# Performance work log

Hardware: AMD Instinct MI355X
Metric: run time of the kernel (lower is better)

Reference implementation:

```python
import jax, jax.numpy as jnp
import numpy as np

N_NODES = 100000
N_EDGES = 1600000
NODE_DIM = 5
HIDDEN = 64
N_LAYERS = 3


def setup_inputs() -> dict:
    key = jax.random.key(0)
    ks = jax.random.split(key, 12)
    s = 0.1
    return {
        "x": jax.random.normal(ks[0], (N_NODES, NODE_DIM), dtype=jnp.float32),
        "edge_index": jax.random.randint(ks[1], (2, N_EDGES), 0, N_NODES, dtype=jnp.int32),
        # message MLP params per layer (stacked over layers)
        "W1": jax.random.normal(ks[2], (N_LAYERS, 2 * NODE_DIM, HIDDEN), dtype=jnp.float32) * s,
        "b1": jnp.zeros((N_LAYERS, HIDDEN), dtype=jnp.float32),
        "W2": jax.random.normal(ks[3], (N_LAYERS, HIDDEN, NODE_DIM), dtype=jnp.float32) * s,
        "b2": jnp.zeros((N_LAYERS, NODE_DIM), dtype=jnp.float32),
        # update MLP params per layer
        "U1": jax.random.normal(ks[4], (N_LAYERS, 2 * NODE_DIM, HIDDEN), dtype=jnp.float32) * s,
        "bu1": jnp.zeros((N_LAYERS, HIDDEN), dtype=jnp.float32),
        "U2": jax.random.normal(ks[5], (N_LAYERS, HIDDEN, NODE_DIM), dtype=jnp.float32) * s,
        "bu2": jnp.zeros((N_LAYERS, NODE_DIM), dtype=jnp.float32),
        # readout
        "Wr": jax.random.normal(ks[6], (NODE_DIM, NODE_DIM), dtype=jnp.float32) * s,
        "br": jnp.zeros((NODE_DIM,), dtype=jnp.float32),
    }


def reference(x, edge_index, W1, b1, W2, b2, U1, bu1, U2, bu2, Wr, br):
    # PyG convention: messages flow from source j = edge_index[0] to target i = edge_index[1]
    src = edge_index[0]
    dst = edge_index[1]
    n = x.shape[0]
    for l in range(N_LAYERS):
        x_i = x[dst]                                   # [E, d] target features
        x_j = x[src]                                   # [E, d] source features
        msg_in = jnp.concatenate([x_i, x_j], axis=-1)  # [E, 2d]
        msg = jax.nn.relu(msg_in @ W1[l] + b1[l]) @ W2[l] + b2[l]   # [E, d]
        aggr = jax.ops.segment_sum(msg, dst, num_segments=n)        # [N, d] scatter-add at targets
        upd_in = jnp.concatenate([x, aggr], axis=-1)   # [N, 2d]
        upd = jax.nn.relu(upd_in @ U1[l] + bu1[l]) @ U2[l] + bu2[l]  # [N, d]
        x = upd + x                                    # residual (in SkeletonGNN.forward)
    return x @ Wr + br
```

## Files before the change

### kernel.cpp

```cpp
#include <hip/hip_runtime.h>

#define N_NODES 100000
#define N_EDGES 1600000
#define DIM 5
#define HID 64
#define N_LAYERS 3
#define SCAN_BLK 256
#define NBLK ((N_NODES + SCAN_BLK - 1) / SCAN_BLK)


__global__ __launch_bounds__(256) void hist_kernel(
    const int* __restrict__ ei, int* __restrict__ cnt, int* __restrict__ rank)
{
    int e = blockIdx.x * blockDim.x + threadIdx.x;
    if (e >= N_EDGES) return;
    int dst = ei[N_EDGES + e];
    rank[e] = atomicAdd(&cnt[dst], 1);
}

__global__ __launch_bounds__(SCAN_BLK) void scan_part_kernel(
    const int* __restrict__ cnt, int* __restrict__ blk_sum)
{
    __shared__ int s[SCAN_BLK];
    int t = threadIdx.x;
    int i = blockIdx.x * SCAN_BLK + t;
    s[t] = (i < N_NODES) ? cnt[i] : 0;
    __syncthreads();
    for (int off = SCAN_BLK / 2; off > 0; off >>= 1) {
        if (t < off) s[t] += s[t + off];
        __syncthreads();
    }
    if (t == 0) blk_sum[blockIdx.x] = s[0];
}

__global__ __launch_bounds__(512) void scan_blk_kernel(
    const int* __restrict__ blk_sum, int* __restrict__ blk_pref)
{
    __shared__ int s[512];
    int t = threadIdx.x;
    int v = (t < NBLK) ? blk_sum[t] : 0;
    s[t] = v;
    __syncthreads();
    for (int off = 1; off < 512; off <<= 1) {
        int a = (t >= off) ? s[t - off] : 0;
        __syncthreads();
        s[t] += a;
        __syncthreads();
    }
    if (t < NBLK) blk_pref[t] = s[t] - v;
}

__global__ __launch_bounds__(SCAN_BLK) void scan_add_kernel(
    const int* __restrict__ cnt, const int* __restrict__ blk_pref,
    int* __restrict__ row_ptr)
{
    __shared__ int s[SCAN_BLK];
    int t = threadIdx.x;
    int i = blockIdx.x * SCAN_BLK + t;
    int c = (i < N_NODES) ? cnt[i] : 0;
    s[t] = c;
    __syncthreads();
    for (int off = 1; off < SCAN_BLK; off <<= 1) {
        int a = (t >= off) ? s[t - off] : 0;
        __syncthreads();
        s[t] += a;
        __syncthreads();
    }
    if (i < N_NODES) row_ptr[i] = blk_pref[blockIdx.x] + s[t] - c;
    if (i == 0) row_ptr[N_NODES] = N_EDGES;
}

__global__ __launch_bounds__(256) void scatter_pair_kernel(
    const int* __restrict__ ei, const int* __restrict__ rank,
    const int* __restrict__ row_ptr, int2* __restrict__ spair)
{
    int e = blockIdx.x * blockDim.x + threadIdx.x;
    if (e >= N_EDGES) return;
    int src = ei[e];
    int dst = ei[N_EDGES + e];
    spair[row_ptr[dst] + rank[e]] = make_int2(src, dst);
}


__global__ __launch_bounds__(256) void edge_msg_sorted_kernel(
    const float* __restrict__ x,
    const int2* __restrict__ spair,
    const float* __restrict__ W1, const float* __restrict__ b1,
    const float* __restrict__ W2, const float* __restrict__ b2,
    float* __restrict__ msg_buf)
{
    int e = blockIdx.x * blockDim.x + threadIdx.x;
    if (e >= N_EDGES) return;
    int2 p = spair[e];

    float in[10];
    const float* xi = x + (long)p.y * DIM;
    const float* xj = x + (long)p.x * DIM;
#pragma unroll
    for (int d = 0; d < DIM; ++d) in[d] = xi[d];
#pragma unroll
    for (int d = 0; d < DIM; ++d) in[DIM + d] = xj[d];

    float msg[DIM];
#pragma unroll
    for (int j = 0; j < DIM; ++j) msg[j] = b2[j];

#pragma unroll 8
    for (int h = 0; h < HID; ++h) {
        float acc = b1[h];
#pragma unroll
        for (int d = 0; d < 10; ++d) acc = fmaf(in[d], W1[d * HID + h], acc);
        acc = fmaxf(acc, 0.0f);
#pragma unroll
        for (int j = 0; j < DIM; ++j) msg[j] = fmaf(acc, W2[h * DIM + j], msg[j]);
    }

    float* mp = msg_buf + (long)e * DIM;
#pragma unroll
    for (int j = 0; j < DIM; ++j) mp[j] = msg[j];
}

template <bool FINAL>
__global__ __launch_bounds__(256) void gather_update8_kernel(
    const float* __restrict__ x,
    const float* __restrict__ msg_buf,
    const int* __restrict__ row_ptr,
    const float* __restrict__ U1, const float* __restrict__ bu1,
    const float* __restrict__ U2, const float* __restrict__ bu2,
    const float* __restrict__ Wr, const float* __restrict__ br,
    float* __restrict__ xout)
{
    int gt = blockIdx.x * blockDim.x + threadIdx.x;
    int v = gt >> 3;
    int r = gt & 7;
    if (v >= N_NODES) return;

    int s = row_ptr[v], e1 = row_ptr[v + 1];

    float agg[DIM] = {0.f, 0.f, 0.f, 0.f, 0.f};
    for (int e = s + r; e < e1; e += 8) {
        const float* mp = msg_buf + (long)e * DIM;
#pragma unroll
        for (int j = 0; j < DIM; ++j) agg[j] += mp[j];
    }
#pragma unroll
    for (int m = 1; m < 8; m <<= 1) {
#pragma unroll
        for (int j = 0; j < DIM; ++j) agg[j] += __shfl_xor(agg[j], m, 64);
    }

    float in2[10];
#pragma unroll
    for (int d = 0; d < DIM; ++d) in2[d] = x[(long)v * DIM + d];
#pragma unroll
    for (int d = 0; d < DIM; ++d) in2[DIM + d] = agg[d];

    float upd[DIM] = {0.f, 0.f, 0.f, 0.f, 0.f};
#pragma unroll
    for (int hh = 0; hh < 8; ++hh) {
        int h = r + hh * 8;
        float acc = bu1[h];
#pragma unroll
        for (int d = 0; d < 10; ++d) acc = fmaf(in2[d], U1[d * HID + h], acc);
        acc = fmaxf(acc, 0.0f);
#pragma unroll
        for (int j = 0; j < DIM; ++j) upd[j] = fmaf(acc, U2[h * DIM + j], upd[j]);
    }
#pragma unroll
    for (int m = 1; m < 8; m <<= 1) {
#pragma unroll
        for (int j = 0; j < DIM; ++j) upd[j] += __shfl_xor(upd[j], m, 64);
    }

    if (r == 0) {
        float xn[DIM];
#pragma unroll
        for (int j = 0; j < DIM; ++j) xn[j] = upd[j] + bu2[j] + in2[j];
        if (FINAL) {
#pragma unroll
            for (int j = 0; j < DIM; ++j) {
                float o = br[j];
#pragma unroll
                for (int d = 0; d < DIM; ++d) o = fmaf(xn[d], Wr[d * DIM + j], o);
                xout[(long)v * DIM + j] = o;
            }
        } else {
#pragma unroll
            for (int j = 0; j < DIM; ++j) xout[(long)v * DIM + j] = xn[j];
        }
    }
}


__global__ __launch_bounds__(256) void edge_msg_kernel(
    const float* __restrict__ x, const int* __restrict__ ei,
    const float* __restrict__ W1, const float* __restrict__ b1,
    const float* __restrict__ W2, const float* __restrict__ b2,
    float* __restrict__ aggr)
{
    int e = blockIdx.x * blockDim.x + threadIdx.x;
    if (e >= N_EDGES) return;
    int src = ei[e];
    int dst = ei[N_EDGES + e];
    float in[10];
    const float* xi = x + (long)dst * DIM;
    const float* xj = x + (long)src * DIM;
#pragma unroll
    for (int d = 0; d < DIM; ++d) in[d] = xi[d];
#pragma unroll
    for (int d = 0; d < DIM; ++d) in[DIM + d] = xj[d];
    float msg[DIM];
#pragma unroll
    for (int j = 0; j < DIM; ++j) msg[j] = b2[j];
#pragma unroll 8
    for (int h = 0; h < HID; ++h) {
        float acc = b1[h];
#pragma unroll
        for (int d = 0; d < 10; ++d) acc = fmaf(in[d], W1[d * HID + h], acc);
        acc = fmaxf(acc, 0.0f);
#pragma unroll
        for (int j = 0; j < DIM; ++j) msg[j] = fmaf(acc, W2[h * DIM + j], msg[j]);
    }
    float* ap = aggr + (long)dst * DIM;
#pragma unroll
    for (int j = 0; j < DIM; ++j) atomicAdd(ap + j, msg[j]);
}

template <bool FINAL>
__global__ __launch_bounds__(256) void node_upd_kernel(
    const float* __restrict__ x, const float* __restrict__ aggr,
    const float* __restrict__ U1, const float* __restrict__ bu1,
    const float* __restrict__ U2, const float* __restrict__ bu2,
    const float* __restrict__ Wr, const float* __restrict__ br,
    float* __restrict__ xout)
{
    int v = blockIdx.x * blockDim.x + threadIdx.x;
    if (v >= N_NODES) return;
    float in[10];
#pragma unroll
    for (int d = 0; d < DIM; ++d) in[d] = x[(long)v * DIM + d];
#pragma unroll
    for (int d = 0; d < DIM; ++d) in[DIM + d] = aggr[(long)v * DIM + d];
    float upd[DIM];
#pragma unroll
    for (int j = 0; j < DIM; ++j) upd[j] = bu2[j];
#pragma unroll 8
    for (int h = 0; h < HID; ++h) {
        float acc = bu1[h];
#pragma unroll
        for (int d = 0; d < 10; ++d) acc = fmaf(in[d], U1[d * HID + h], acc);
        acc = fmaxf(acc, 0.0f);
#pragma unroll
        for (int j = 0; j < DIM; ++j) upd[j] = fmaf(acc, U2[h * DIM + j], upd[j]);
    }
    float xn[DIM];
#pragma unroll
    for (int j = 0; j < DIM; ++j) xn[j] = upd[j] + in[j];
    if (FINAL) {
#pragma unroll
        for (int j = 0; j < DIM; ++j) {
            float o = br[j];
#pragma unroll
            for (int d = 0; d < DIM; ++d) o = fmaf(xn[d], Wr[d * DIM + j], o);
            xout[(long)v * DIM + j] = o;
        }
    } else {
#pragma unroll
        for (int j = 0; j < DIM; ++j) xout[(long)v * DIM + j] = xn[j];
    }
}


static inline size_t alignup(size_t x) { return (x + 255) & ~(size_t)255; }

extern "C" void kernel_launch(void* const* d_in, const int* in_sizes, int n_in,
                              void* d_out, int out_size, void* d_ws, size_t ws_size,
                              hipStream_t stream) {
    const float* x   = (const float*)d_in[0];
    const int*   ei  = (const int*)d_in[1];
    const float* W1  = (const float*)d_in[2];
    const float* b1  = (const float*)d_in[3];
    const float* W2  = (const float*)d_in[4];
    const float* b2  = (const float*)d_in[5];
    const float* U1  = (const float*)d_in[6];
    const float* bu1 = (const float*)d_in[7];
    const float* U2  = (const float*)d_in[8];
    const float* bu2 = (const float*)d_in[9];
    const float* Wr  = (const float*)d_in[10];
    const float* br  = (const float*)d_in[11];
    float* out = (float*)d_out;

    char* ws = (char*)d_ws;

    size_t o_cnt  = 0;
    size_t o_row  = alignup(o_cnt + (size_t)N_NODES * 4);
    size_t o_bsum = alignup(o_row + (size_t)(N_NODES + 1) * 4);
    size_t o_bpre = alignup(o_bsum + (size_t)NBLK * 4);
    size_t o_sp   = alignup(o_bpre + (size_t)NBLK * 4);
    size_t o_xA   = alignup(o_sp + (size_t)N_EDGES * 8);
    size_t o_xB   = alignup(o_xA + (size_t)N_NODES * DIM * 4);
    size_t o_msg  = alignup(o_xB + (size_t)N_NODES * DIM * 4);
    size_t needed = o_msg + (size_t)N_EDGES * DIM * 4;

    dim3 blk(256);
    dim3 eg((N_EDGES + 255) / 256);
    dim3 ng((N_NODES + 255) / 256);
    dim3 ng8((N_NODES * 8 + 255) / 256);

    if (ws_size < needed) {
        size_t nbytes = (size_t)N_NODES * DIM * sizeof(float);
        float* aggr = (float*)ws;
        float* xA   = (float*)(ws + nbytes);
        float* xB   = (float*)(ws + 2 * nbytes);
        const float* xcur = x;
        for (int l = 0; l < N_LAYERS; ++l) {
            hipMemsetAsync(aggr, 0, nbytes, stream);
            edge_msg_kernel<<<eg, blk, 0, stream>>>(
                xcur, ei, W1 + l * 10 * HID, b1 + l * HID,
                W2 + l * HID * DIM, b2 + l * DIM, aggr);
            if (l < N_LAYERS - 1) {
                float* xn = (l == 0) ? xA : xB;
                node_upd_kernel<false><<<ng, blk, 0, stream>>>(
                    xcur, aggr, U1 + l * 10 * HID, bu1 + l * HID,
                    U2 + l * HID * DIM, bu2 + l * DIM, Wr, br, xn);
                xcur = xn;
            } else {
                node_upd_kernel<true><<<ng, blk, 0, stream>>>(
                    xcur, aggr, U1 + l * 10 * HID, bu1 + l * HID,
                    U2 + l * HID * DIM, bu2 + l * DIM, Wr, br, out);
            }
        }
        return;
    }

    int* cnt      = (int*)(ws + o_cnt);
    int* row_ptr  = (int*)(ws + o_row);
    int* blk_sum  = (int*)(ws + o_bsum);
    int* blk_pref = (int*)(ws + o_bpre);
    int2* spair   = (int2*)(ws + o_sp);
    float* xA     = (float*)(ws + o_xA);
    float* xB     = (float*)(ws + o_xB);
    float* msgbuf = (float*)(ws + o_msg);
    int* rank     = (int*)(ws + o_msg);

    hipMemsetAsync(cnt, 0, (size_t)N_NODES * 4, stream);
    hist_kernel<<<eg, blk, 0, stream>>>(ei, cnt, rank);
    scan_part_kernel<<<NBLK, SCAN_BLK, 0, stream>>>(cnt, blk_sum);
    scan_blk_kernel<<<1, 512, 0, stream>>>(blk_sum, blk_pref);
    scan_add_kernel<<<NBLK, SCAN_BLK, 0, stream>>>(cnt, blk_pref, row_ptr);
    scatter_pair_kernel<<<eg, blk, 0, stream>>>(ei, rank, row_ptr, spair);

    const float* xcur = x;
    for (int l = 0; l < N_LAYERS; ++l) {
        edge_msg_sorted_kernel<<<eg, blk, 0, stream>>>(
            xcur, spair, W1 + l * 10 * HID, b1 + l * HID,
            W2 + l * HID * DIM, b2 + l * DIM, msgbuf);
        if (l < N_LAYERS - 1) {
            float* xn = (l == 0) ? xA : xB;
            gather_update8_kernel<false><<<ng8, blk, 0, stream>>>(
                xcur, msgbuf, row_ptr, U1 + l * 10 * HID, bu1 + l * HID,
                U2 + l * HID * DIM, bu2 + l * DIM, Wr, br, xn);
            xcur = xn;
        } else {
            gather_update8_kernel<true><<<ng8, blk, 0, stream>>>(
                xcur, msgbuf, row_ptr, U1 + l * 10 * HID, bu1 + l * HID,
                U2 + l * HID * DIM, bu2 + l * DIM, Wr, br, out);
        }
    }
}
```

Before: 386.1 us.

## Fuse layer-0 message computation into histogram pass with permuted gather

```diff
diff --git a/kernel.cpp b/kernel.cpp
--- a/kernel.cpp
+++ b/kernel.cpp
@@ -8,15 +8,50 @@
 #define SCAN_BLK 256
 #define NBLK ((N_NODES + SCAN_BLK - 1) / SCAN_BLK)
 
-
-__global__ __launch_bounds__(256) void hist_kernel(
-    const int* __restrict__ ei, int* __restrict__ cnt, int* __restrict__ rank)
+__global__ __launch_bounds__(256) void fused_hist_msg1_kernel(
+    const float* __restrict__ x,
+    const int* __restrict__ ei,
+    const float* __restrict__ W1, const float* __restrict__ b1,
+    const float* __restrict__ W2, const float* __restrict__ b2,
+    int* __restrict__ cnt, int* __restrict__ rank,
+    float* __restrict__ msg0)
 {
     int e = blockIdx.x * blockDim.x + threadIdx.x;
     if (e >= N_EDGES) return;
+    int src = ei[e];
     int dst = ei[N_EDGES + e];
-    rank[e] = atomicAdd(&cnt[dst], 1);
-}
+
+    int rk = atomicAdd(&cnt[dst], 1);
+
+    float in[10];
+    const float* xi = x + (long)dst * DIM;
+    const float* xj = x + (long)src * DIM;
+#pragma unroll
+    for (int d = 0; d < DIM; ++d) in[d] = xi[d];
+#pragma unroll
+    for (int d = 0; d < DIM; ++d) in[DIM + d] = xj[d];
+
+    float msg[DIM];
+#pragma unroll
+    for (int j = 0; j < DIM; ++j) msg[j] = b2[j];
+
+#pragma unroll 8
+    for (int h = 0; h < HID; ++h) {
+        float acc = b1[h];
+#pragma unroll
+        for (int d = 0; d < 10; ++d) acc = fmaf(in[d], W1[d * HID + h], acc);
+        acc = fmaxf(acc, 0.0f);
+#pragma unroll
+        for (int j = 0; j < DIM; ++j) msg[j] = fmaf(acc, W2[h * DIM + j], msg[j]);
+    }
+
+    float* mp = msg0 + (long)e * DIM;
+#pragma unroll
+    for (int j = 0; j < DIM; ++j) mp[j] = msg[j];
+
+    rank[e] = rk;
+}
+
 
 __global__ __launch_bounds__(SCAN_BLK) void scan_part_kernel(
     const int* __restrict__ cnt, int* __restrict__ blk_sum)
@@ -70,15 +105,18 @@
     if (i == 0) row_ptr[N_NODES] = N_EDGES;
 }
 
-__global__ __launch_bounds__(256) void scatter_pair_kernel(
+__global__ __launch_bounds__(256) void scatter_pair_perm_kernel(
     const int* __restrict__ ei, const int* __restrict__ rank,
-    const int* __restrict__ row_ptr, int2* __restrict__ spair)
+    const int* __restrict__ row_ptr,
+    int2* __restrict__ spair, int* __restrict__ eperm)
 {
     int e = blockIdx.x * blockDim.x + threadIdx.x;
     if (e >= N_EDGES) return;
     int src = ei[e];
     int dst = ei[N_EDGES + e];
-    spair[row_ptr[dst] + rank[e]] = make_int2(src, dst);
+    int pos = row_ptr[dst] + rank[e];
+    spair[pos] = make_int2(src, dst);
+    eperm[pos] = e;
 }
 
 
@@ -120,10 +158,11 @@
     for (int j = 0; j < DIM; ++j) mp[j] = msg[j];
 }
 
-template <bool FINAL>
+template <bool FINAL, bool INDIRECT>
 __global__ __launch_bounds__(256) void gather_update8_kernel(
     const float* __restrict__ x,
     const float* __restrict__ msg_buf,
+    const int* __restrict__ eperm,
     const int* __restrict__ row_ptr,
     const float* __restrict__ U1, const float* __restrict__ bu1,
     const float* __restrict__ U2, const float* __restrict__ bu2,
@@ -139,7 +178,8 @@
 
     float agg[DIM] = {0.f, 0.f, 0.f, 0.f, 0.f};
     for (int e = s + r; e < e1; e += 8) {
-        const float* mp = msg_buf + (long)e * DIM;
+        long me = INDIRECT ? (long)eperm[e] : (long)e;
+        const float* mp = msg_buf + me * DIM;
 #pragma unroll
         for (int j = 0; j < DIM; ++j) agg[j] += mp[j];
     }
@@ -297,7 +337,9 @@
     size_t o_bsum = alignup(o_row + (size_t)(N_NODES + 1) * 4);
     size_t o_bpre = alignup(o_bsum + (size_t)NBLK * 4);
     size_t o_sp   = alignup(o_bpre + (size_t)NBLK * 4);
-    size_t o_xA   = alignup(o_sp + (size_t)N_EDGES * 8);
+    size_t o_perm = alignup(o_sp + (size_t)N_EDGES * 8);
+    size_t o_rank = alignup(o_perm + (size_t)N_EDGES * 4);
+    size_t o_xA   = alignup(o_rank + (size_t)N_EDGES * 4);
     size_t o_xB   = alignup(o_xA + (size_t)N_NODES * DIM * 4);
     size_t o_msg  = alignup(o_xB + (size_t)N_NODES * DIM * 4);
     size_t needed = o_msg + (size_t)N_EDGES * DIM * 4;
@@ -338,33 +380,35 @@
     int* blk_sum  = (int*)(ws + o_bsum);
     int* blk_pref = (int*)(ws + o_bpre);
     int2* spair   = (int2*)(ws + o_sp);
+    int* eperm    = (int*)(ws + o_perm);
+    int* rank     = (int*)(ws + o_rank);
     float* xA     = (float*)(ws + o_xA);
     float* xB     = (float*)(ws + o_xB);
     float* msgbuf = (float*)(ws + o_msg);
-    int* rank     = (int*)(ws + o_msg);
 
     hipMemsetAsync(cnt, 0, (size_t)N_NODES * 4, stream);
-    hist_kernel<<<eg, blk, 0, stream>>>(ei, cnt, rank);
+    fused_hist_msg1_kernel<<<eg, blk, 0, stream>>>(
+        x, ei, W1, b1, W2, b2, cnt, rank, msgbuf);
+
     scan_part_kernel<<<NBLK, SCAN_BLK, 0, stream>>>(cnt, blk_sum);
     scan_blk_kernel<<<1, 512, 0, stream>>>(blk_sum, blk_pref);
     scan_add_kernel<<<NBLK, SCAN_BLK, 0, stream>>>(cnt, blk_pref, row_ptr);
-    scatter_pair_kernel<<<eg, blk, 0, stream>>>(ei, rank, row_ptr, spair);
-
-    const float* xcur = x;
-    for (int l = 0; l < N_LAYERS; ++l) {
-        edge_msg_sorted_kernel<<<eg, blk, 0, stream>>>(
-            xcur, spair, W1 + l * 10 * HID, b1 + l * HID,
-            W2 + l * HID * DIM, b2 + l * DIM, msgbuf);
-        if (l < N_LAYERS - 1) {
-            float* xn = (l == 0) ? xA : xB;
-            gather_update8_kernel<false><<<ng8, blk, 0, stream>>>(
-                xcur, msgbuf, row_ptr, U1 + l * 10 * HID, bu1 + l * HID,
-                U2 + l * HID * DIM, bu2 + l * DIM, Wr, br, xn);
-            xcur = xn;
-        } else {
-            gather_update8_kernel<true><<<ng8, blk, 0, stream>>>(
-                xcur, msgbuf, row_ptr, U1 + l * 10 * HID, bu1 + l * HID,
-                U2 + l * HID * DIM, bu2 + l * DIM, Wr, br, out);
-        }
-    }
-}
+    scatter_pair_perm_kernel<<<eg, blk, 0, stream>>>(ei, rank, row_ptr, spair, eperm);
+
+    gather_update8_kernel<false, true><<<ng8, blk, 0, stream>>>(
+        x, msgbuf, eperm, row_ptr, U1, bu1, U2, bu2, Wr, br, xA);
+
+    edge_msg_sorted_kernel<<<eg, blk, 0, stream>>>(
+        xA, spair, W1 + 10 * HID, b1 + HID,
+        W2 + HID * DIM, b2 + DIM, msgbuf);
+    gather_update8_kernel<false, false><<<ng8, blk, 0, stream>>>(
+        xA, msgbuf, nullptr, row_ptr, U1 + 10 * HID, bu1 + HID,
+        U2 + HID * DIM, bu2 + DIM, Wr, br, xB);
+
+    edge_msg_sorted_kernel<<<eg, blk, 0, stream>>>(
+        xB, spair, W1 + 2 * 10 * HID, b1 + 2 * HID,
+        W2 + 2 * HID * DIM, b2 + 2 * DIM, msgbuf);
+    gather_update8_kernel<true, false><<<ng8, blk, 0, stream>>>(
+        xB, msgbuf, nullptr, row_ptr, U1 + 2 * 10 * HID, bu1 + 2 * HID,
+        U2 + 2 * HID * DIM, bu2 + 2 * DIM, Wr, br, out);
+}
```

New measurement: 388.1 us. Within noise of the previous version (+0.5%).
